# Kernel optimization log

Hardware: AMD Instinct MI355X
Metric: run time of the kernel (lower is better)

## Reference

```python
import jax, jax.numpy as jnp
import numpy as np

N_DIM = 512
HIDDEN = 512


def setup_inputs() -> dict:
    key = jax.random.key(0)
    ks = jax.random.split(key, 9)
    s = 0.02
    x = jax.random.normal(ks[0], (4, 4096, N_DIM), dtype=jnp.float32)
    Wq = jax.random.normal(ks[1], (N_DIM, HIDDEN), dtype=jnp.float32) * s
    bq = jnp.zeros((HIDDEN,), dtype=jnp.float32)
    Wk = jax.random.normal(ks[2], (N_DIM, HIDDEN), dtype=jnp.float32) * s
    bk = jnp.zeros((HIDDEN,), dtype=jnp.float32)
    Wv = jax.random.normal(ks[3], (N_DIM, HIDDEN), dtype=jnp.float32) * s
    bv = jnp.zeros((HIDDEN,), dtype=jnp.float32)
    Wo = jax.random.normal(ks[4], (HIDDEN, N_DIM), dtype=jnp.float32) * s
    bo = jnp.zeros((N_DIM,), dtype=jnp.float32)
    return {"x": x, "Wq": Wq, "bq": bq, "Wk": Wk, "bk": bk,
            "Wv": Wv, "bv": bv, "Wo": Wo, "bo": bo}


def reference(x, Wq, bq, Wk, bk, Wv, bv, Wo, bo):
    # x: [B, S, n_dim]
    q = jnp.einsum('bsd,dh->bsh', x, Wq) + bq  # [B,S,H]
    k = jnp.einsum('bsd,dh->bsh', x, Wk) + bk
    v = jnp.einsum('bsd,dh->bsh', x, Wv) + bv
    # NOTE: original module uses UNSCALED scores (no 1/sqrt(d))
    scores = jnp.einsum('bqh,bkh->bqk', q, k)  # [B,S,S]
    attn = jax.nn.softmax(scores, axis=-1)
    y = jnp.einsum('bqk,bkh->bqh', attn, v)
    return jnp.einsum('bsh,hd->bsd', y, Wo) + bo
```

## Files before the change

### kernel.cpp

```cpp
#include <hip/hip_runtime.h>
#include <hip/hip_bf16.h>

typedef _Float16 h8 __attribute__((ext_vector_type(8)));
typedef __bf16   b8 __attribute__((ext_vector_type(8)));
typedef float    f4 __attribute__((ext_vector_type(4)));

#define B_    4
#define S_    4096
#define D_    512
#define ROWS_ (B_ * S_)
#define NQKV_ 1536
#define BR    64
#define BC    32
#define KP    520
#define PP    40
#define NIT   (S_ / BC)
#define MSH   (30.0f * 1.4426950408889634f)
#define L2E   1.4426950408889634f

__device__ __forceinline__ void gl_lds16(const void* src, void* dst) {
    __builtin_amdgcn_global_load_lds(
        (const __attribute__((address_space(1))) unsigned int*)src,
        (__attribute__((address_space(3))) unsigned int*)dst, 16, 0, 0);
}

__global__ __launch_bounds__(256) void convert_all(
    const float* __restrict__ x,
    const float* __restrict__ Wq, const float* __restrict__ Wk, const float* __restrict__ Wv,
    const float* __restrict__ bq, const float* __restrict__ bk, const float* __restrict__ bv,
    const float* __restrict__ Wo,
    _Float16* __restrict__ xh, _Float16* __restrict__ wqkvT, _Float16* __restrict__ woT,
    float* __restrict__ bqkv)
{
    long i0 = (long)blockIdx.x * blockDim.x + threadIdx.x;
    long stride = (long)gridDim.x * blockDim.x;
    const long NX  = (long)ROWS_ * D_;
    const long NW  = (long)D_ * NQKV_;
    const long NWO = (long)D_ * D_;

    for (long i = i0; i < NX; i += stride) xh[i] = (_Float16)x[i];

    for (long i = i0; i < NW; i += stride) {
        long n = i >> 9, k = i & 511;
        long which = n >> 9, nn = n & 511;
        const float* W = (which == 0) ? Wq : (which == 1) ? Wk : Wv;
        wqkvT[i] = (_Float16)W[k * 512 + nn];
    }
    for (long i = i0; i < NWO; i += stride) {
        long n = i >> 9, k = i & 511;
        woT[i] = (_Float16)Wo[k * 512 + n];
    }
    for (long i = i0; i < NQKV_; i += stride) {
        long which = i >> 9, nn = i & 511;
        const float* bb = (which == 0) ? bq : (which == 1) ? bk : bv;
        bqkv[i] = bb[nn];
    }
}

#define GP 40
template <bool OUT_F16>
__global__ __launch_bounds__(256) void gemm_bt(
    const _Float16* __restrict__ A, const _Float16* __restrict__ BT,
    const float* __restrict__ bias, void* __restrict__ Cout,
    int M, int N, int K)
{
    __shared__ _Float16 As[128 * GP];
    __shared__ _Float16 Bs[128 * GP];

    int tid = threadIdx.x;
    int w = tid >> 6, lane = tid & 63, quad = lane >> 4, l16 = lane & 15;
    long row0 = (long)blockIdx.x * 128, col0 = (long)blockIdx.y * 128;
    int wr = (w >> 1) * 64, wc = (w & 1) * 64;

    f4 acc[4][4];
    for (int i = 0; i < 4; i++)
        for (int j = 0; j < 4; j++) acc[i][j] = (f4){0.f, 0.f, 0.f, 0.f};

    int sr = tid >> 1, sc = (tid & 1) * 16;
    for (int k0 = 0; k0 < K; k0 += 32) {
        __syncthreads();
        {
            const h8* ga = (const h8*)(A  + (row0 + sr) * K + k0 + sc);
            const h8* gb = (const h8*)(BT + (col0 + sr) * K + k0 + sc);
            *(h8*)(As + sr * GP + sc)     = ga[0];
            *(h8*)(As + sr * GP + sc + 8) = ga[1];
            *(h8*)(Bs + sr * GP + sc)     = gb[0];
            *(h8*)(Bs + sr * GP + sc + 8) = gb[1];
        }
        __syncthreads();
        h8 af[4], bf[4];
        for (int i = 0; i < 4; i++) af[i] = *(const h8*)(As + (wr + i * 16 + l16) * GP + quad * 8);
        for (int j = 0; j < 4; j++) bf[j] = *(const h8*)(Bs + (wc + j * 16 + l16) * GP + quad * 8);
        for (int i = 0; i < 4; i++)
            for (int j = 0; j < 4; j++)
                acc[i][j] = __builtin_amdgcn_mfma_f32_16x16x32_f16(af[i], bf[j], acc[i][j], 0, 0, 0);
    }
    for (int i = 0; i < 4; i++)
        for (int j = 0; j < 4; j++)
            for (int r = 0; r < 4; r++) {
                long row = row0 + wr + i * 16 + quad * 4 + r;
                long col = col0 + wc + j * 16 + l16;
                float v = acc[i][j][r] + bias[col];
                if (OUT_F16) ((_Float16*)Cout)[row * N + col] = (_Float16)v;
                else         ((float*)Cout)[row * N + col]    = v;
            }
}

__global__ __launch_bounds__(256) void pack_v(const _Float16* __restrict__ qkv,
                                              __bf16* __restrict__ vP)
{
    __shared__ _Float16 T[32 * 520];
    int kt = blockIdx.x, b = blockIdx.y;
    int t = threadIdx.x;

    const _Float16* src = qkv + ((long)b * S_ + kt * 32 + (t >> 3)) * NQKV_ + 1024;
#pragma unroll
    for (int i = 0; i < 8; i++) {
        int c = (t & 7) + i * 8;
        *(h8*)(T + (t >> 3) * 520 + c * 8) = *(const h8*)(src + c * 8);
    }
    __syncthreads();

    __bf16* dst = vP + (((long)b * 128 + kt) * 32) * 512;
#pragma unroll
    for (int i = 0; i < 8; i++) {
        int c = t + i * 256;
        int dt = c >> 6, q = (c >> 4) & 3, l = c & 15;
        b8 out;
#pragma unroll
        for (int k3 = 0; k3 < 8; k3++)
            out[k3] = (__bf16)(float)T[(q * 8 + k3) * 520 + dt * 16 + l];
        *(b8*)(dst + (long)c * 8) = out;
    }
}

__global__ __launch_bounds__(512, 2) void attn_kernel(const _Float16* __restrict__ qkv,
                                                      const __bf16* __restrict__ vP,
                                                      _Float16* __restrict__ yb)
{
    __shared__ _Float16 Ks[2][BC * KP];
    __shared__ __bf16   Ps[2][BR * PP];
    __shared__ float    lpart[2][BR];

    const int tid = threadIdx.x;
    const int w = tid >> 6, lane = tid & 63, quad = lane >> 4, l16 = lane & 15;
    const int rs = (w & 3) * 16;
    const int kh = w >> 2;
    const int b = blockIdx.y;
    const long q0 = (long)blockIdx.x * BR;
    const long rowBase = (long)b * S_;

    const _Float16* kbase = qkv + rowBase * NQKV_ + 512;

#pragma unroll
    for (int i = 0; i < 4; i++) {
        int r = w * 4 + i;
        gl_lds16(kbase + (long)r * NQKV_ + lane * 8, Ks[0] + r * KP);
    }

    const __bf16* vpbase = vP + ((long)b * 128 * 32 + w * 4) * 512 + lane * 8;

    h8 Qf[16];
    {
        const _Float16* qrow = qkv + (rowBase + q0 + rs + l16) * NQKV_;
#pragma unroll
        for (int ks = 0; ks < 16; ks++)
            Qf[ks] = *(const h8*)(qrow + ks * 32 + quad * 8);
    }

    f4 O[4][4];
#pragma unroll
    for (int rt = 0; rt < 4; rt++)
#pragma unroll
        for (int ct = 0; ct < 4; ct++) O[rt][ct] = (f4){0.f, 0.f, 0.f, 0.f};
    float lo[4] = {0.f, 0.f, 0.f, 0.f};

    __syncthreads();

    for (int kt = 0; kt < NIT; kt++) {
        const int cur = kt & 1, nxt = cur ^ 1;

        if (kt + 1 < NIT) {
            const _Float16* kn = kbase + (long)(kt + 1) * BC * NQKV_;
#pragma unroll
            for (int i = 0; i < 4; i++) {
                int r = w * 4 + i;
                gl_lds16(kn + (long)r * NQKV_ + lane * 8, Ks[nxt] + r * KP);
            }
        }
        b8 vreg[4];
        {
            const __bf16* vs = vpbase + (long)kt * (32 * 512);
#pragma unroll
            for (int ct = 0; ct < 4; ct++)
                vreg[ct] = *(const b8*)(vs + ct * 512);
        }

        f4 S0 = (f4){0.f, 0.f, 0.f, 0.f};
        f4 S1 = (f4){0.f, 0.f, 0.f, 0.f};
        const _Float16* krow = Ks[cur] + (kh * 16 + l16) * KP + quad * 8;
#pragma unroll
        for (int ks = 0; ks < 8; ks++) {
            h8 kb0 = *(const h8*)(krow + ks * 32);
            h8 kb1 = *(const h8*)(krow + (ks + 8) * 32);
            S0 = __builtin_amdgcn_mfma_f32_16x16x32_f16(Qf[ks],     kb0, S0, 0, 0, 0);
            S1 = __builtin_amdgcn_mfma_f32_16x16x32_f16(Qf[ks + 8], kb1, S1, 0, 0, 0);
        }

#pragma unroll
        for (int r = 0; r < 4; r++) {
            float p = exp2f((S0[r] + S1[r]) * L2E - MSH);
            __bf16 pb = (__bf16)p;
            Ps[cur][(rs + quad * 4 + r) * PP + kh * 16 + l16] = pb;
            lo[r] += (float)pb;
        }

        __syncthreads();

        b8 pa[4];
#pragma unroll
        for (int rt = 0; rt < 4; rt++)
            pa[rt] = *(const b8*)(Ps[cur] + (rt * 16 + l16) * PP + quad * 8);
#pragma unroll
        for (int ct = 0; ct < 4; ct++)
#pragma unroll
            for (int rt = 0; rt < 4; rt++)
                O[rt][ct] = __builtin_amdgcn_mfma_f32_16x16x32_bf16(pa[rt], vreg[ct], O[rt][ct], 0, 0, 0);
    }

#pragma unroll
    for (int r = 0; r < 4; r++)
#pragma unroll
        for (int m = 1; m < 16; m <<= 1) lo[r] += __shfl_xor(lo[r], m, 16);
    if (l16 == 0)
        for (int r = 0; r < 4; r++) lpart[kh][rs + quad * 4 + r] = lo[r];
    __syncthreads();

    for (int rt = 0; rt < 4; rt++) {
        f4 l0 = *(const f4*)(&lpart[0][rt * 16 + quad * 4]);
        f4 l1 = *(const f4*)(&lpart[1][rt * 16 + quad * 4]);
        float li[4];
        for (int r = 0; r < 4; r++) li[r] = 1.f / (l0[r] + l1[r]);
        for (int ct = 0; ct < 4; ct++)
            for (int r = 0; r < 4; r++) {
                long row = rowBase + q0 + rt * 16 + quad * 4 + r;
                long col = w * 64 + ct * 16 + l16;
                yb[row * 512 + col] = (_Float16)(O[rt][ct][r] * li[r]);
            }
    }
}

extern "C" void kernel_launch(void* const* d_in, const int* in_sizes, int n_in,
                              void* d_out, int out_size, void* d_ws, size_t ws_size,
                              hipStream_t stream)
{
    const float* x  = (const float*)d_in[0];
    const float* Wq = (const float*)d_in[1];
    const float* bq = (const float*)d_in[2];
    const float* Wk = (const float*)d_in[3];
    const float* bk = (const float*)d_in[4];
    const float* Wv = (const float*)d_in[5];
    const float* bv = (const float*)d_in[6];
    const float* Wo = (const float*)d_in[7];
    const float* bo = (const float*)d_in[8];
    float* out = (float*)d_out;

    char* ws = (char*)d_ws;
    _Float16* xh    = (_Float16*)(ws);
    _Float16* qkv   = (_Float16*)(ws + 16777216);
    __bf16*   vP    = (__bf16*)(ws + 67108864);
    _Float16* yb    = (_Float16*)(ws + 83886080);
    _Float16* wqkvT = (_Float16*)(ws + 100663296);
    _Float16* woT   = (_Float16*)(ws + 102236160);
    float*    bqkv  = (float*)(ws + 102760448);

    convert_all<<<2048, 256, 0, stream>>>(x, Wq, Wk, Wv, bq, bk, bv, Wo,
                                          xh, wqkvT, woT, bqkv);

    dim3 g1(128, 12);
    gemm_bt<true><<<g1, 256, 0, stream>>>(xh, wqkvT, bqkv, qkv, ROWS_, NQKV_, D_);

    dim3 gp(128, 4);
    pack_v<<<gp, 256, 0, stream>>>(qkv, vP);

    dim3 ga(64, 4);
    attn_kernel<<<ga, 512, 0, stream>>>(qkv, vP, yb);

    dim3 g2(128, 4);
    gemm_bt<false><<<g2, 256, 0, stream>>>(yb, woT, bo, out, ROWS_, D_, D_);
}
```

Baseline: 347.2 us.

## Deepen attention K/V prefetch with 4-slot LDS ring and register double-buffer

Grows the K tile ring in LDS from 2 to 4 slots and prefetches K two iterations ahead. V fragments are now double-buffered in registers and loaded one iteration ahead. The loop is unrolled by two, and __syncthreads is replaced with explicit vmcnt/lgkmcnt waits plus s_barrier, so the wait covers only the tile about to be consumed. The aim is to hide global and LDS-DMA latency behind the MFMA work. In exchange, LDS use per block roughly doubles, which likely drops occupancy from two blocks per CU to one, and the V double-buffer raises register pressure.

Result: faster. 340.1 us (-2.0%).

```diff
diff --git a/kernel.cpp b/kernel.cpp
--- a/kernel.cpp
+++ b/kernel.cpp
@@ -15,6 +15,7 @@
 #define KP    520
 #define PP    40
 #define NIT   (S_ / BC)
+#define KTILE (BC * KP)
 #define MSH   (30.0f * 1.4426950408889634f)
 #define L2E   1.4426950408889634f
 
@@ -138,8 +139,8 @@
                                                       const __bf16* __restrict__ vP,
                                                       _Float16* __restrict__ yb)
 {
-    __shared__ _Float16 Ks[2][BC * KP];
-    __shared__ __bf16   Ps[2][BR * PP];
+    __shared__ _Float16 Ks[4 * KTILE];
+    __shared__ __bf16   Ps[2 * BR * PP];
     __shared__ float    lpart[2][BR];
 
     const int tid = threadIdx.x;
@@ -151,13 +152,6 @@
     const long rowBase = (long)b * S_;
 
     const _Float16* kbase = qkv + rowBase * NQKV_ + 512;
-
-#pragma unroll
-    for (int i = 0; i < 4; i++) {
-        int r = w * 4 + i;
-        gl_lds16(kbase + (long)r * NQKV_ + lane * 8, Ks[0] + r * KP);
-    }
-
     const __bf16* vpbase = vP + ((long)b * 128 * 32 + w * 4) * 512 + lane * 8;
 
     h8 Qf[16];
@@ -168,6 +162,19 @@
             Qf[ks] = *(const h8*)(qrow + ks * 32 + quad * 8);
     }
 
+#pragma unroll
+    for (int t = 0; t < 2; t++)
+#pragma unroll
+        for (int i = 0; i < 4; i++) {
+            int r = w * 4 + i;
+            gl_lds16(kbase + (long)(t * BC + r) * NQKV_ + lane * 8,
+                     Ks + t * KTILE + r * KP);
+        }
+    b8 vA[4], vB[4];
+#pragma unroll
+    for (int ct = 0; ct < 4; ct++)
+        vA[ct] = *(const b8*)(vpbase + ct * 512);
+
     f4 O[4][4];
 #pragma unroll
     for (int rt = 0; rt < 4; rt++)
@@ -175,58 +182,72 @@
         for (int ct = 0; ct < 4; ct++) O[rt][ct] = (f4){0.f, 0.f, 0.f, 0.f};
     float lo[4] = {0.f, 0.f, 0.f, 0.f};
 
-    __syncthreads();
-
-    for (int kt = 0; kt < NIT; kt++) {
-        const int cur = kt & 1, nxt = cur ^ 1;
-
-        if (kt + 1 < NIT) {
-            const _Float16* kn = kbase + (long)(kt + 1) * BC * NQKV_;
-#pragma unroll
-            for (int i = 0; i < 4; i++) {
-                int r = w * 4 + i;
-                gl_lds16(kn + (long)r * NQKV_ + lane * 8, Ks[nxt] + r * KP);
-            }
-        }
-        b8 vreg[4];
-        {
-            const __bf16* vs = vpbase + (long)kt * (32 * 512);
-#pragma unroll
-            for (int ct = 0; ct < 4; ct++)
-                vreg[ct] = *(const b8*)(vs + ct * 512);
-        }
-
-        f4 S0 = (f4){0.f, 0.f, 0.f, 0.f};
-        f4 S1 = (f4){0.f, 0.f, 0.f, 0.f};
-        const _Float16* krow = Ks[cur] + (kh * 16 + l16) * KP + quad * 8;
-#pragma unroll
-        for (int ks = 0; ks < 8; ks++) {
-            h8 kb0 = *(const h8*)(krow + ks * 32);
-            h8 kb1 = *(const h8*)(krow + (ks + 8) * 32);
-            S0 = __builtin_amdgcn_mfma_f32_16x16x32_f16(Qf[ks],     kb0, S0, 0, 0, 0);
-            S1 = __builtin_amdgcn_mfma_f32_16x16x32_f16(Qf[ks + 8], kb1, S1, 0, 0, 0);
-        }
-
-#pragma unroll
-        for (int r = 0; r < 4; r++) {
-            float p = exp2f((S0[r] + S1[r]) * L2E - MSH);
-            __bf16 pb = (__bf16)p;
-            Ps[cur][(rs + quad * 4 + r) * PP + kh * 16 + l16] = pb;
-            lo[r] += (float)pb;
-        }
-
-        __syncthreads();
-
-        b8 pa[4];
-#pragma unroll
-        for (int rt = 0; rt < 4; rt++)
-            pa[rt] = *(const b8*)(Ps[cur] + (rt * 16 + l16) * PP + quad * 8);
-#pragma unroll
-        for (int ct = 0; ct < 4; ct++)
-#pragma unroll
-            for (int rt = 0; rt < 4; rt++)
-                O[rt][ct] = __builtin_amdgcn_mfma_f32_16x16x32_bf16(pa[rt], vreg[ct], O[rt][ct], 0, 0, 0);
-    }
+    __builtin_amdgcn_sched_barrier(0);
+    asm volatile("s_waitcnt vmcnt(8)");
+    __builtin_amdgcn_s_barrier();
+    __builtin_amdgcn_sched_barrier(0);
+
+#define ATTN_BODY(KT, VUSE, VLOAD)                                              \
+  {                                                                             \
+    const int kt_ = (KT);                                                       \
+           \
+    if (kt_ + 1 < NIT) {                                                        \
+      const __bf16* vs = vpbase + (long)(kt_ + 1) * (32 * 512);                 \
+      _Pragma("unroll")                                                         \
+      for (int ct = 0; ct < 4; ct++)                                            \
+        VLOAD[ct] = *(const b8*)(vs + ct * 512);                                \
+    }                                                                           \
+    if (kt_ + 2 < NIT) {                                                        \
+      const _Float16* kn = kbase + (long)(kt_ + 2) * BC * NQKV_;                \
+      _Float16* kd = Ks + ((kt_ + 2) & 3) * KTILE;                              \
+      _Pragma("unroll")                                                         \
+      for (int i = 0; i < 4; i++) {                                             \
+        int r = w * 4 + i;                                                      \
+        gl_lds16(kn + (long)r * NQKV_ + lane * 8, kd + r * KP);                 \
+      }                                                                         \
+    }                                                                           \
+                  \
+    f4 S0 = (f4){0.f, 0.f, 0.f, 0.f};                                           \
+    f4 S1 = (f4){0.f, 0.f, 0.f, 0.f};                                           \
+    const _Float16* krow = Ks + (kt_ & 3) * KTILE + (kh * 16 + l16) * KP + quad * 8; \
+    _Pragma("unroll")                                                           \
+    for (int ks = 0; ks < 8; ks++) {                                            \
+      h8 kb0 = *(const h8*)(krow + ks * 32);                                    \
+      h8 kb1 = *(const h8*)(krow + (ks + 8) * 32);                              \
+      S0 = __builtin_amdgcn_mfma_f32_16x16x32_f16(Qf[ks],     kb0, S0, 0, 0, 0);\
+      S1 = __builtin_amdgcn_mfma_f32_16x16x32_f16(Qf[ks + 8], kb1, S1, 0, 0, 0);\
+    }                                                                           \
+    __bf16* ps = Ps + (kt_ & 1) * (BR * PP);                                    \
+    _Pragma("unroll")                                                           \
+    for (int r = 0; r < 4; r++) {                                               \
+      float p = exp2f((S0[r] + S1[r]) * L2E - MSH);                             \
+      __bf16 pb = (__bf16)p;                                                    \
+      ps[(rs + quad * 4 + r) * PP + kh * 16 + l16] = pb;                        \
+      lo[r] += (float)pb;                                                       \
+    }                                                                           \
+    __builtin_amdgcn_sched_barrier(0);                                          \
+    if (kt_ < NIT - 2)       asm volatile("s_waitcnt vmcnt(8)");                \
+    else if (kt_ == NIT - 2) asm volatile("s_waitcnt vmcnt(4)");                \
+    asm volatile("s_waitcnt lgkmcnt(0)");                                       \
+    __builtin_amdgcn_s_barrier();                                               \
+    __builtin_amdgcn_sched_barrier(0);                                          \
+           \
+    b8 pa[4];                                                                   \
+    _Pragma("unroll")                                                           \
+    for (int rt = 0; rt < 4; rt++)                                              \
+      pa[rt] = *(const b8*)(ps + (rt * 16 + l16) * PP + quad * 8);              \
+    _Pragma("unroll")                                                           \
+    for (int ct = 0; ct < 4; ct++)                                              \
+      _Pragma("unroll")                                                         \
+      for (int rt = 0; rt < 4; rt++)                                            \
+        O[rt][ct] = __builtin_amdgcn_mfma_f32_16x16x32_bf16(pa[rt], VUSE[ct], O[rt][ct], 0, 0, 0); \
+  }
+
+    for (int kt = 0; kt < NIT; kt += 2) {
+        ATTN_BODY(kt,     vA, vB);
+        ATTN_BODY(kt + 1, vB, vA);
+    }
+#undef ATTN_BODY
 
 #pragma unroll
     for (int r = 0; r < 4; r++)
```
